# Kernel tuning notes

Hardware: AMD Instinct MI355X
Metric: run time of the kernel (lower is better)

Reference implementation:

```python
import jax, jax.numpy as jnp
import numpy as np

TAU = 0.1


def setup_inputs() -> dict:
    key = jax.random.key(0)
    k1, k2, k3 = jax.random.split(key, 3)
    B, C, H, W = 32, 1, 512, 512
    input1 = jax.random.normal(k1, (B, C, H, W), dtype=jnp.float32)
    input2 = jax.random.normal(k2, (B, C, H, W), dtype=jnp.float32)
    mask = jax.random.uniform(k3, (B, C, H, W), dtype=jnp.float32)
    return {"input1": input1, "input2": input2, "mask": mask}


def reference(input1, input2, mask):
    # logit=True: apply sigmoid first
    x1 = jax.nn.sigmoid(input1)
    x2 = jax.nn.sigmoid(input2)
    B = x1.shape[0]
    N = x1.shape[1] * x1.shape[2] * x1.shape[3]

    # positive similarity: masked MSE per sample over (C,H,W)
    sim_pos = jnp.exp(-jnp.mean((mask * (x1 - x2)) ** 2, axis=(1, 2, 3)) / TAU)

    # negative similarities: all-pairs MSE via GEMM expansion trick
    # mean((a-b)^2) = (|a|^2 + |b|^2 - 2 a.b) / N
    f1 = x1.reshape(B, N)
    f2 = x2.reshape(B, N)
    sq1 = jnp.sum(f1 * f1, axis=1)  # [B]
    sq2 = jnp.sum(f2 * f2, axis=1)  # [B]
    cross = f1 @ f2.T               # [B,B]
    d = (sq1[:, None] + sq2[None, :] - 2.0 * cross) / N
    sim = jnp.exp(-d / TAU)         # [B,B]
    # exclude b1 == b2 diagonal terms
    sim_neg = jnp.sum(sim, axis=1) - jnp.diagonal(sim)

    loss = -jnp.log(sim_pos / (sim_pos + sim_neg))
    return jnp.mean(loss)
```

## Files before the change

kernel.cpp:

```cpp
#include <hip/hip_runtime.h>
#include <hip/hip_bf16.h>

#define NF 262144
#define NROWS 32
#define CSTRIDE 1088
#define NKG 16

#define PAN1_OFF 0
#define PAN2_OFF 4194304
#define CREC_OFF 8388608
#define WS2_OFF  (CREC_OFF + 1024 * CSTRIDE)
#define PQ_OFF   (WS2_OFF + NKG * CSTRIDE)

typedef __attribute__((ext_vector_type(8))) __bf16 bf16x8;
typedef __attribute__((ext_vector_type(4))) __bf16 bf16x4;
typedef __attribute__((ext_vector_type(16))) float f32x16;

__device__ __forceinline__ float sigmoid_fast(float x) {
    float e = __expf(-x);
    return __builtin_amdgcn_rcpf(1.0f + e);
}

__device__ __forceinline__ void gload16(const void* g, const float* l) {
    __builtin_amdgcn_global_load_lds(
        (const __attribute__((address_space(1))) void*)g,
        (__attribute__((address_space(3))) void*)l, 16, 0, 0);
}

__global__ __launch_bounds__(256) void cl_pack(const float* __restrict__ in1,
                                               const float* __restrict__ in2,
                                               const float* __restrict__ msk,
                                               float* __restrict__ ws) {
    const int tid = threadIdx.x;
    const int r   = blockIdx.x >> 4;
    const int s   = blockIdx.x & 15;

    const size_t base = (size_t)r * NF + (size_t)s * 16384;
    const float4* p1 = (const float4*)(in1 + base);
    const float4* p2 = (const float4*)(in2 + base);
    const float4* pm = (const float4*)(msk + base);
    char* panel1 = (char*)(ws + PAN1_OFF);
    char* panel2 = (char*)(ws + PAN2_OFF);

    float pos = 0.0f, q1 = 0.0f, q2 = 0.0f;

    #pragma unroll
    for (int rd = 0; rd < 4; ++rd) {
        const int o = rd * 1024;
        float4 A[4], B[4], M[4];
        #pragma unroll
        for (int j = 0; j < 4; ++j) A[j] = p1[o + j * 256 + tid];
        #pragma unroll
        for (int j = 0; j < 4; ++j) B[j] = p2[o + j * 256 + tid];
        #pragma unroll
        for (int j = 0; j < 4; ++j) M[j] = pm[o + j * 256 + tid];

        #pragma unroll
        for (int j = 0; j < 4; ++j) {
            const float* xa = (const float*)&A[j];
            const float* xb = (const float*)&B[j];
            const float* xm = (const float*)&M[j];
            bf16x4 ua, ub;
            #pragma unroll
            for (int e = 0; e < 4; ++e) {
                float sa = sigmoid_fast(xa[e]);
                float sb = sigmoid_fast(xb[e]);
                float d  = xm[e] * (sa - sb);
                pos = fmaf(d, d, pos);
                q1  = fmaf(sa, sa, q1);
                q2  = fmaf(sb, sb, q2);
                ua[e] = (__bf16)sa;
                ub[e] = (__bf16)sb;
            }
            const size_t k = base + (size_t)rd * 4096 + (size_t)j * 1024 + tid * 4;
            *(bf16x4*)(panel1 + k * 2) = ua;
            *(bf16x4*)(panel2 + k * 2) = ub;
        }
    }

    __shared__ float sred[4][3];
    #pragma unroll
    for (int off = 32; off; off >>= 1) {
        pos += __shfl_xor(pos, off);
        q1  += __shfl_xor(q1, off);
        q2  += __shfl_xor(q2, off);
    }
    if ((tid & 63) == 0) {
        sred[tid >> 6][0] = pos; sred[tid >> 6][1] = q1; sred[tid >> 6][2] = q2;
    }
    __syncthreads();
    if (tid == 0) {
        float* PQ = ws + PQ_OFF;
        PQ[r * 16 + s]        = sred[0][0] + sred[1][0] + sred[2][0] + sred[3][0];
        PQ[512 + r * 16 + s]  = sred[0][1] + sred[1][1] + sred[2][1] + sred[3][1];
        PQ[1024 + r * 16 + s] = sred[0][2] + sred[1][2] + sred[2][2] + sred[3][2];
    }
}

__global__ __launch_bounds__(256) void cl_gemm(const float* __restrict__ ws_ro,
                                               float* __restrict__ ws) {
    __shared__ float smem[4096];

    const int tid  = threadIdx.x;
    const int w    = tid >> 6;
    const int lane = tid & 63;
    const int r    = lane & 31;
    const int g    = lane >> 5;

    const char* pan[2] = {(const char*)(ws_ro + PAN1_OFF), (const char*)(ws_ro + PAN2_OFF)};
    const int kt0 = blockIdx.x * 4;

    f32x16 acc;
    #pragma unroll
    for (int k = 0; k < 16; ++k) acc[k] = 0.0f;

    auto stage = [&](int p, int kt) {
        #pragma unroll
        for (int m = 0; m < 2; ++m) {
            const int n   = w * 2 + m;
            const int a   = n >> 2;
            const int row = (n & 3) * 8 + (lane >> 3);
            const int sc  = (lane & 7) ^ (row & 7);
            gload16(pan[a] + ((size_t)row * NF + (size_t)kt * 64) * 2 + sc * 16,
                    smem + p * 2048 + n * 256);
        }
    };

    auto compute = [&](int p) {
        const int cs = (w * 2 + g) ^ (r & 7);
        const float* base = smem + p * 2048 + r * 32 + cs * 4;
        bf16x8 fa = *(const bf16x8*)(base);
        bf16x8 fb = *(const bf16x8*)(base + 1024);
        acc = __builtin_amdgcn_mfma_f32_32x32x16_bf16(fa, fb, acc, 0, 0, 0);
    };

    stage(0, kt0);
    __syncthreads();
    #pragma unroll
    for (int t = 0; t < 3; ++t) {
        stage((t + 1) & 1, kt0 + t + 1);
        compute(t & 1);
        __syncthreads();
    }
    compute(1);
    __syncthreads();

    const int col = lane & 31;
    const int rhi = (lane >> 5) * 4;
    #pragma unroll
    for (int reg = 0; reg < 16; ++reg) {
        const int row = (reg & 3) + 8 * (reg >> 2) + rhi;
        smem[w * 1024 + row * 32 + col] = acc[reg];
    }
    __syncthreads();

    float* P = ws + CREC_OFF + (size_t)blockIdx.x * CSTRIDE;
    for (int idx = tid; idx < 1024; idx += 256)
        P[idx] = smem[idx] + smem[1024 + idx] + smem[2048 + idx] + smem[3072 + idx];
}

__global__ __launch_bounds__(256) void cl_reduce(const float* __restrict__ ws_ro,
                                                 float* __restrict__ ws) {
    const int kg   = blockIdx.x >> 2;
    const int slot = (blockIdx.x & 3) * 256 + threadIdx.x;
    const float* base = ws_ro + CREC_OFF + (size_t)kg * 64 * CSTRIDE + slot;
    float s = 0.0f;
    #pragma unroll 8
    for (int k = 0; k < 64; ++k) s += base[(size_t)k * CSTRIDE];
    ws[WS2_OFF + kg * CSTRIDE + slot] = s;
}

__global__ __launch_bounds__(1024) void cl_final(const float* __restrict__ ws,
                                                 float* __restrict__ out) {
    __shared__ float s_loss[32];
    const int tid = threadIdx.x;
    const int i = tid >> 5, j = tid & 31;
    const float invN = 1.0f / (float)NF;

    float c = 0.0f, p = 0.0f, s1 = 0.0f, s2 = 0.0f;
    #pragma unroll
    for (int k = 0; k < NKG; ++k)
        c += ws[WS2_OFF + (size_t)k * CSTRIDE + i * 32 + j];
    const float* PQ = ws + PQ_OFF;
    #pragma unroll
    for (int k = 0; k < 16; ++k) {
        p  += PQ[i * 16 + k];
        s1 += PQ[512 + i * 16 + k];
        s2 += PQ[1024 + j * 16 + k];
    }

    float d = (s1 + s2 - 2.0f * c) * invN;
    float sim = (i == j) ? 0.0f : expf(-d * 10.0f);
    #pragma unroll
    for (int off = 16; off; off >>= 1) sim += __shfl_xor(sim, off);

    if (j == 0) {
        float sp = expf(-p * invN * 10.0f);
        s_loss[i] = -logf(sp / (sp + sim));
    }
    __syncthreads();
    if (tid == 0) {
        float t = 0.0f;
        #pragma unroll
        for (int k = 0; k < 32; ++k) t += s_loss[k];
        out[0] = t * (1.0f / 32.0f);
    }
}

extern "C" void kernel_launch(void* const* d_in, const int* in_sizes, int n_in,
                              void* d_out, int out_size, void* d_ws, size_t ws_size,
                              hipStream_t stream) {
    const float* in1 = (const float*)d_in[0];
    const float* in2 = (const float*)d_in[1];
    const float* msk = (const float*)d_in[2];
    float* out = (float*)d_out;
    float* ws  = (float*)d_ws;

    cl_pack  <<<512,  256, 0, stream>>>(in1, in2, msk, ws);
    cl_gemm  <<<1024, 256, 0, stream>>>(ws, ws);
    cl_reduce<<<64,   256, 0, stream>>>(ws, ws);
    cl_final <<<1,   1024, 0, stream>>>(ws, out);
}
```

Baseline: 43.37 us.

## Split fused pack into per-input sigmoid kernels and a separate masked-MSE kernel

Replaces the single pack kernel, which streamed both inputs and the mask together, with three kernels. Two of them apply sigmoid to one input each, writing its bf16 panel and sum of squares. The third rereads both bf16 panels alongside the mask to compute the positive masked MSE. Panel 2 and the GEMM partial-result area are also shifted by a few KB, to avoid address aliasing between the two panels in the GEMM loads. The split lowers per-thread register and stream pressure, but adds two kernel launches and an extra read of both panels. The positive term is now computed from bf16-rounded sigmoids instead of fp32 ones.

Result: slower. 53.99 us (+24.5%).

```diff
diff --git a/kernel.cpp b/kernel.cpp
--- a/kernel.cpp
+++ b/kernel.cpp
@@ -7,8 +7,8 @@
 #define NKG 16
 
 #define PAN1_OFF 0
-#define PAN2_OFF 4194304
-#define CREC_OFF 8388608
+#define PAN2_OFF (4194304 + 1088)
+#define CREC_OFF (8388608 + 2176)
 #define WS2_OFF  (CREC_OFF + 1024 * CSTRIDE)
 #define PQ_OFF   (WS2_OFF + NKG * CSTRIDE)
 
@@ -27,74 +27,91 @@
         (__attribute__((address_space(3))) void*)l, 16, 0, 0);
 }
 
-__global__ __launch_bounds__(256) void cl_pack(const float* __restrict__ in1,
-                                               const float* __restrict__ in2,
-                                               const float* __restrict__ msk,
-                                               float* __restrict__ ws) {
+__global__ __launch_bounds__(256) void cl_sig(const float* __restrict__ in,
+                                              char* __restrict__ panel,
+                                              float* __restrict__ qout) {
     const int tid = threadIdx.x;
-    const int r   = blockIdx.x >> 4;
-    const int s   = blockIdx.x & 15;
-
-    const size_t base = (size_t)r * NF + (size_t)s * 16384;
-    const float4* p1 = (const float4*)(in1 + base);
-    const float4* p2 = (const float4*)(in2 + base);
-    const float4* pm = (const float4*)(msk + base);
-    char* panel1 = (char*)(ws + PAN1_OFF);
-    char* panel2 = (char*)(ws + PAN2_OFF);
-
-    float pos = 0.0f, q1 = 0.0f, q2 = 0.0f;
-
-    #pragma unroll
-    for (int rd = 0; rd < 4; ++rd) {
+    const int r   = blockIdx.x >> 5;
+    const int s   = blockIdx.x & 31;
+
+    const size_t base = (size_t)r * NF + (size_t)s * 8192;
+    const float4* p = (const float4*)(in + base);
+
+    float q = 0.0f;
+
+    #pragma unroll
+    for (int rd = 0; rd < 2; ++rd) {
         const int o = rd * 1024;
-        float4 A[4], B[4], M[4];
-        #pragma unroll
-        for (int j = 0; j < 4; ++j) A[j] = p1[o + j * 256 + tid];
-        #pragma unroll
-        for (int j = 0; j < 4; ++j) B[j] = p2[o + j * 256 + tid];
-        #pragma unroll
-        for (int j = 0; j < 4; ++j) M[j] = pm[o + j * 256 + tid];
+        float4 V[4];
+        #pragma unroll
+        for (int j = 0; j < 4; ++j) V[j] = p[o + j * 256 + tid];
 
         #pragma unroll
         for (int j = 0; j < 4; ++j) {
-            const float* xa = (const float*)&A[j];
-            const float* xb = (const float*)&B[j];
-            const float* xm = (const float*)&M[j];
-            bf16x4 ua, ub;
+            const float* x = (const float*)&V[j];
+            bf16x4 u;
             #pragma unroll
             for (int e = 0; e < 4; ++e) {
-                float sa = sigmoid_fast(xa[e]);
-                float sb = sigmoid_fast(xb[e]);
-                float d  = xm[e] * (sa - sb);
+                float sa = sigmoid_fast(x[e]);
+                q = fmaf(sa, sa, q);
+                u[e] = (__bf16)sa;
+            }
+            const size_t k = base + (size_t)(o + j * 256 + tid) * 4;
+            *(bf16x4*)(panel + k * 2) = u;
+        }
+    }
+
+    __shared__ float sred[4];
+    #pragma unroll
+    for (int off = 32; off; off >>= 1) q += __shfl_xor(q, off);
+    if ((tid & 63) == 0) sred[tid >> 6] = q;
+    __syncthreads();
+    if (tid == 0) qout[r * 32 + s] = sred[0] + sred[1] + sred[2] + sred[3];
+}
+
+__global__ __launch_bounds__(256) void cl_pos(const float* __restrict__ msk,
+                                              const char* __restrict__ pan1,
+                                              const char* __restrict__ pan2,
+                                              float* __restrict__ posout) {
+    const int tid = threadIdx.x;
+    const int r   = blockIdx.x >> 5;
+    const int s   = blockIdx.x & 31;
+
+    const size_t base = (size_t)r * NF + (size_t)s * 8192;
+    const float4* pm = (const float4*)(msk + base);
+
+    float pos = 0.0f;
+
+    #pragma unroll
+    for (int rd = 0; rd < 2; ++rd) {
+        const int o = rd * 1024;
+        float4 M[4];
+        bf16x4 U1[4], U2[4];
+        #pragma unroll
+        for (int j = 0; j < 4; ++j) M[j] = pm[o + j * 256 + tid];
+        #pragma unroll
+        for (int j = 0; j < 4; ++j) {
+            const size_t eo = (base + (size_t)(o + j * 256 + tid) * 4) * 2;
+            U1[j] = *(const bf16x4*)(pan1 + eo);
+            U2[j] = *(const bf16x4*)(pan2 + eo);
+        }
+        #pragma unroll
+        for (int j = 0; j < 4; ++j) {
+            const float* m = (const float*)&M[j];
+            #pragma unroll
+            for (int e = 0; e < 4; ++e) {
+                float d = m[e] * ((float)U1[j][e] - (float)U2[j][e]);
                 pos = fmaf(d, d, pos);
-                q1  = fmaf(sa, sa, q1);
-                q2  = fmaf(sb, sb, q2);
-                ua[e] = (__bf16)sa;
-                ub[e] = (__bf16)sb;
             }
-            const size_t k = base + (size_t)rd * 4096 + (size_t)j * 1024 + tid * 4;
-            *(bf16x4*)(panel1 + k * 2) = ua;
-            *(bf16x4*)(panel2 + k * 2) = ub;
-        }
-    }
-
-    __shared__ float sred[4][3];
-    #pragma unroll
-    for (int off = 32; off; off >>= 1) {
-        pos += __shfl_xor(pos, off);
-        q1  += __shfl_xor(q1, off);
-        q2  += __shfl_xor(q2, off);
-    }
-    if ((tid & 63) == 0) {
-        sred[tid >> 6][0] = pos; sred[tid >> 6][1] = q1; sred[tid >> 6][2] = q2;
-    }
-    __syncthreads();
-    if (tid == 0) {
-        float* PQ = ws + PQ_OFF;
-        PQ[r * 16 + s]        = sred[0][0] + sred[1][0] + sred[2][0] + sred[3][0];
-        PQ[512 + r * 16 + s]  = sred[0][1] + sred[1][1] + sred[2][1] + sred[3][1];
-        PQ[1024 + r * 16 + s] = sred[0][2] + sred[1][2] + sred[2][2] + sred[3][2];
-    }
+        }
+    }
+
+    __shared__ float sred[4];
+    #pragma unroll
+    for (int off = 32; off; off >>= 1) pos += __shfl_xor(pos, off);
+    if ((tid & 63) == 0) sred[tid >> 6] = pos;
+    __syncthreads();
+    if (tid == 0) posout[r * 32 + s] = sred[0] + sred[1] + sred[2] + sred[3];
 }
 
 __global__ __launch_bounds__(256) void cl_gemm(const float* __restrict__ ws_ro,
@@ -183,10 +200,10 @@
         c += ws[WS2_OFF + (size_t)k * CSTRIDE + i * 32 + j];
     const float* PQ = ws + PQ_OFF;
     #pragma unroll
-    for (int k = 0; k < 16; ++k) {
-        p  += PQ[i * 16 + k];
-        s1 += PQ[512 + i * 16 + k];
-        s2 += PQ[1024 + j * 16 + k];
+    for (int k = 0; k < 32; ++k) {
+        p  += PQ[i * 32 + k];
+        s1 += PQ[1024 + i * 32 + k];
+        s2 += PQ[2048 + j * 32 + k];
     }
 
     float d = (s1 + s2 - 2.0f * c) * invN;
@@ -216,7 +233,13 @@
     float* out = (float*)d_out;
     float* ws  = (float*)d_ws;
 
-    cl_pack  <<<512,  256, 0, stream>>>(in1, in2, msk, ws);
+    char* pan1 = (char*)(ws + PAN1_OFF);
+    char* pan2 = (char*)(ws + PAN2_OFF);
+    float* PQ  = ws + PQ_OFF;
+
+    cl_sig   <<<1024, 256, 0, stream>>>(in1, pan1, PQ + 1024);
+    cl_sig   <<<1024, 256, 0, stream>>>(in2, pan2, PQ + 2048);
+    cl_pos   <<<1024, 256, 0, stream>>>(msk, pan1, pan2, PQ);
     cl_gemm  <<<1024, 256, 0, stream>>>(ws, ws);
     cl_reduce<<<64,   256, 0, stream>>>(ws, ws);
     cl_final <<<1,   1024, 0, stream>>>(ws, out);
```
